# Kernel tuning notes

Measured on AMD Instinct MI355X. Metric: run time of the kernel, lower is better.

## Reference

```python
import jax, jax.numpy as jnp
import numpy as np

B, S, D, H, L, V = 2, 2048, 768, 12, 2, 32000
DH = D // H
DF = 4 * D
LN_EPS = 1e-5


def _pos_enc():
    # faithful to source: exponent uses 2*i/D with i already stepping by 2
    pos = jnp.arange(S, dtype=jnp.float32)[:, None]
    i = jnp.arange(0, D, 2, dtype=jnp.float32)
    ang = pos / (10000.0 ** (2.0 * i / D))
    enc = jnp.zeros((S, D), jnp.float32)
    enc = enc.at[:, 0::2].set(jnp.sin(ang)).at[:, 1::2].set(jnp.cos(ang))
    return enc


def _ln(x, g, b):
    m = jnp.mean(x, axis=-1, keepdims=True)
    v = jnp.mean((x - m) ** 2, axis=-1, keepdims=True)
    return (x - m) / jnp.sqrt(v + LN_EPS) * g + b


def _layer(x, p):
    Wq, bq, Wk, bk, Wv, bv, Wo, bo, g1, be1, W1, b1, W2, b2, g2, be2 = p
    q = (x @ Wq + bq).reshape(B, S, H, DH)
    k = (x @ Wk + bk).reshape(B, S, H, DH)
    v = (x @ Wv + bv).reshape(B, S, H, DH)
    # NOTE: source divides by sqrt(embed_dim), not sqrt(head_dim)
    attn = jnp.einsum('bqhd,bkhd->bhqk', q, k) / jnp.sqrt(jnp.float32(D))
    attn = jax.nn.softmax(attn, axis=-1)  # [B,H,S,S]
    o = jnp.einsum('bhqk,bkhd->bqhd', attn, v).reshape(B, S, D)
    o = o @ Wo + bo
    x = _ln(x + o, g1, be1)
    h = jax.nn.gelu(x @ W1 + b1, approximate=False)
    x = _ln(x + h @ W2 + b2, g2, be2)
    return x


def setup_inputs() -> dict:
    key = jax.random.key(0)
    ks = jax.random.split(key, 16)
    n = lambda k, shape: jax.random.normal(k, shape, dtype=jnp.float32) * 0.02
    return {
        'input_ids': jax.random.randint(ks[0], (B, S), 0, V),
        'embed_table': n(ks[1], (V, D)),
        'Wq': n(ks[2], (L, D, D)), 'bq': jnp.zeros((L, D), jnp.float32),
        'Wk': n(ks[3], (L, D, D)), 'bk': jnp.zeros((L, D), jnp.float32),
        'Wv': n(ks[4], (L, D, D)), 'bv': jnp.zeros((L, D), jnp.float32),
        'Wo': n(ks[5], (L, D, D)), 'bo': jnp.zeros((L, D), jnp.float32),
        'ln1_g': jnp.ones((L, D), jnp.float32), 'ln1_b': jnp.zeros((L, D), jnp.float32),
        'W1': n(ks[6], (L, D, DF)), 'b1': jnp.zeros((L, DF), jnp.float32),
        'W2': n(ks[7], (L, DF, D)), 'b2': jnp.zeros((L, D), jnp.float32),
        'ln2_g': jnp.ones((L, D), jnp.float32), 'ln2_b': jnp.zeros((L, D), jnp.float32),
        'Wd': n(ks[8], (D, D)), 'bd': jnp.zeros((D,), jnp.float32),
        'lnm_g': jnp.ones((D,), jnp.float32), 'lnm_b': jnp.zeros((D,), jnp.float32),
        'dec_b': jnp.zeros((V,), jnp.float32),
    }


def reference(input_ids, embed_table, Wq, bq, Wk, bk, Wv, bv, Wo, bo,
              ln1_g, ln1_b, W1, b1, W2, b2, ln2_g, ln2_b,
              Wd, bd, lnm_g, lnm_b, dec_b):
    x = embed_table[input_ids] + _pos_enc()[None]  # [B,S,D]

    def step(h, p):
        return _layer(h, p), None

    x, _ = jax.lax.scan(step, x, (Wq, bq, Wk, bk, Wv, bv, Wo, bo,
                                  ln1_g, ln1_b, W1, b1, W2, b2, ln2_g, ln2_b))
    # MLM head with decoder weight tied to embedding table
    h = jax.nn.gelu(x @ Wd + bd, approximate=False)
    h = _ln(h, lnm_g, lnm_b)
    return h @ embed_table.T + dec_b  # [B,S,V]
```

## Files before the change

kernel.cpp:

```cpp
#include <hip/hip_runtime.h>
#include <hip/hip_bf16.h>
#include <cstdint>

typedef __bf16 bf16x8 __attribute__((ext_vector_type(8)));
typedef float  f32x4  __attribute__((ext_vector_type(4)));
typedef unsigned short u16;
typedef u16 u16x8 __attribute__((ext_vector_type(8)));

__device__ __forceinline__ u16 f2bf(float f) {
    union { float f; uint32_t u; } x{f};
    uint32_t u = x.u;
    return (u16)((u + 0x7fffu + ((u >> 16) & 1u)) >> 16);
}

__device__ __forceinline__ float gelu_f(float x) {
    return 0.5f * x * (1.0f + erff(x * 0.70710678118654752f));
}

__device__ __forceinline__ void gl_lds16(const void* g, void* l) {
    __builtin_amdgcn_global_load_lds(
        (__attribute__((address_space(1))) void*)(void*)g,
        (__attribute__((address_space(3))) void*)l, 16, 0, 0);
}

#define MFMA16(a, b, c) __builtin_amdgcn_mfma_f32_16x16x32_bf16((a), (b), (c), 0, 0, 0)
#define SB0 __builtin_amdgcn_sched_barrier(0)

template<int EPI, int OUTF32, int LOC, int SPLITK>
__global__ __launch_bounds__(256, 2) void gemm_bf16(
    const u16* __restrict__ A, const u16* __restrict__ Bt,
    const float* __restrict__ bias, void* __restrict__ Cout,
    int N_, int K_)
{
    __shared__ u16 lA[128 * 64];
    __shared__ u16 lB[128 * 64];
    const int tid  = threadIdx.x;
    const int lane = tid & 63;
    const int wave = tid >> 6;
    const int wr = wave >> 1, wc = wave & 1;
    long row0, col0;
    if (LOC) {
        const int bid = blockIdx.x;
        const int chunk = bid >> 9, rem = bid & 511;
        row0 = (long)(rem & 31) * 128;
        col0 = (long)(chunk * 16 + (rem >> 5)) * 128;
    } else {
        row0 = (long)blockIdx.y * 128;
        col0 = (long)blockIdx.x * 128;
    }
    const int KS = K_ / SPLITK;
    const int kz = (SPLITK > 1) ? blockIdx.z * KS : 0;

    f32x4 acc[4][4];
#pragma unroll
    for (int i = 0; i < 4; ++i)
#pragma unroll
        for (int j = 0; j < 4; ++j)
#pragma unroll
            for (int t = 0; t < 4; ++t) acc[i][j][t] = 0.f;

    int sRow[4], sKb[4];
#pragma unroll
    for (int t = 0; t < 4; ++t) {
        int byteoff = (wave * 4 + t) * 1024 + lane * 16;
        int r = byteoff >> 7;
        sRow[t] = r;
        sKb[t]  = (byteoff & 127) ^ ((r & 7) << 4);
    }
    const int laneRC = lane & 15;
    const int laneK2 = (lane >> 4) * 16;

    for (int k0 = kz; k0 < kz + KS; k0 += 64) {
#pragma unroll
        for (int t = 0; t < 4; ++t) {
            const int cb = (wave * 4 + t) * 1024;
            gl_lds16(A  + (row0 + sRow[t]) * K_ + k0 + (sKb[t] >> 1), (char*)lA + cb);
            gl_lds16(Bt + (col0 + sRow[t]) * K_ + k0 + (sKb[t] >> 1), (char*)lB + cb);
        }
        __syncthreads();
#pragma unroll
        for (int kk = 0; kk < 2; ++kk) {
            bf16x8 af[4], bfr[4];
#pragma unroll
            for (int i = 0; i < 4; ++i) {
                int r = wr * 64 + i * 16 + laneRC;
                af[i] = *(const bf16x8*)((const char*)lA + r * 128 + ((kk * 64 + laneK2) ^ ((r & 7) << 4)));
            }
#pragma unroll
            for (int j = 0; j < 4; ++j) {
                int n = wc * 64 + j * 16 + laneRC;
                bfr[j] = *(const bf16x8*)((const char*)lB + n * 128 + ((kk * 64 + laneK2) ^ ((n & 7) << 4)));
            }
#pragma unroll
            for (int i = 0; i < 4; ++i)
#pragma unroll
                for (int j = 0; j < 4; ++j)
                    acc[i][j] = MFMA16(af[i], bfr[j], acc[i][j]);
        }
        __syncthreads();
    }

    float* outF = (float*)Cout + (SPLITK > 1 ? (long)blockIdx.z * 4096 * N_ : 0);
#pragma unroll
    for (int j = 0; j < 4; ++j) {
        const long cidx = col0 + wc * 64 + j * 16 + laneRC;
        const float bvv = (SPLITK == 1 || blockIdx.z == 0) ? bias[cidx] : 0.f;
#pragma unroll
        for (int i = 0; i < 4; ++i) {
            const long rbase = row0 + wr * 64 + i * 16 + ((lane >> 4) << 2);
#pragma unroll
            for (int t = 0; t < 4; ++t) {
                float v = acc[i][j][t] + bvv;
                if (EPI) v = gelu_f(v);
                const long off = (rbase + t) * N_ + cidx;
                if (OUTF32) outF[off] = v;
                else        ((u16*)Cout)[off] = f2bf(v);
            }
        }
    }
}

template<int EPI, int OUTF32>
__global__ __launch_bounds__(256, 4) void gemm64(
    const u16* __restrict__ A, const u16* __restrict__ Bt,
    const float* __restrict__ bias, void* __restrict__ Cout,
    int N_, int K_)
{
    __shared__ u16 lA[64 * 64];
    __shared__ u16 lB[64 * 64];
    const int tid  = threadIdx.x;
    const int lane = tid & 63;
    const int wave = tid >> 6;
    const int wr = wave >> 1, wc = wave & 1;
    const long row0 = (long)blockIdx.y * 64;
    const long col0 = (long)blockIdx.x * 64;

    f32x4 acc[2][2];
#pragma unroll
    for (int i = 0; i < 2; ++i)
#pragma unroll
        for (int j = 0; j < 2; ++j)
#pragma unroll
            for (int t = 0; t < 4; ++t) acc[i][j][t] = 0.f;

    int sRow[2], sKb[2];
#pragma unroll
    for (int t = 0; t < 2; ++t) {
        int byteoff = (wave * 2 + t) * 1024 + lane * 16;
        int r = byteoff >> 7;
        sRow[t] = r;
        sKb[t]  = (byteoff & 127) ^ ((r & 7) << 4);
    }
    const int laneRC = lane & 15;
    const int laneK2 = (lane >> 4) * 16;

    for (int k0 = 0; k0 < K_; k0 += 64) {
#pragma unroll
        for (int t = 0; t < 2; ++t) {
            const int cb = (wave * 2 + t) * 1024;
            gl_lds16(A  + (row0 + sRow[t]) * K_ + k0 + (sKb[t] >> 1), (char*)lA + cb);
            gl_lds16(Bt + (col0 + sRow[t]) * K_ + k0 + (sKb[t] >> 1), (char*)lB + cb);
        }
        __syncthreads();
#pragma unroll
        for (int kk = 0; kk < 2; ++kk) {
            bf16x8 af[2], bfr[2];
#pragma unroll
            for (int i = 0; i < 2; ++i) {
                int r = wr * 32 + i * 16 + laneRC;
                af[i] = *(const bf16x8*)((const char*)lA + r * 128 + ((kk * 64 + laneK2) ^ ((r & 7) << 4)));
            }
#pragma unroll
            for (int j = 0; j < 2; ++j) {
                int n = wc * 32 + j * 16 + laneRC;
                bfr[j] = *(const bf16x8*)((const char*)lB + n * 128 + ((kk * 64 + laneK2) ^ ((n & 7) << 4)));
            }
#pragma unroll
            for (int i = 0; i < 2; ++i)
#pragma unroll
                for (int j = 0; j < 2; ++j)
                    acc[i][j] = MFMA16(af[i], bfr[j], acc[i][j]);
        }
        __syncthreads();
    }

#pragma unroll
    for (int j = 0; j < 2; ++j) {
        const long cidx = col0 + wc * 32 + j * 16 + laneRC;
        const float bvv = bias[cidx];
#pragma unroll
        for (int i = 0; i < 2; ++i) {
            const long rbase = row0 + wr * 32 + i * 16 + ((lane >> 4) << 2);
#pragma unroll
            for (int t = 0; t < 4; ++t) {
                float v = acc[i][j][t] + bvv;
                if (EPI) v = gelu_f(v);
                const long off = (rbase + t) * N_ + cidx;
                if (OUTF32) ((float*)Cout)[off] = v;
                else        ((u16*)Cout)[off]  = f2bf(v);
            }
        }
    }
}

__global__ __launch_bounds__(256, 3) void attn_fwd(
    const u16* __restrict__ qkv, u16* __restrict__ outb, float scale)
{
    __shared__ u16 lQ[64 * 64];
    __shared__ u16 lK[2][64 * 64];
    __shared__ u16 lVt[2][64 * 64];
    __shared__ u16 lP[64 * 64];
    const int bh = blockIdx.x;
    const int b = bh / 12, h = bh % 12;
    const int q0 = blockIdx.y * 64;
    const int tid = threadIdx.x, lane = tid & 63, wave = tid >> 6;
    const long baseQ = (long)b * 2048 * 2304 + h * 64;
    const long baseK = baseQ + 768;
    const long baseV = baseQ + 1536;
    const int laneRC = lane & 15;
    const int laneK2 = (lane >> 4) * 16;

    int stR[2], stC[2];
#pragma unroll
    for (int t = 0; t < 2; ++t) {
        const int byteoff = (wave * 2 + t) * 1024 + lane * 16;
        const int r = byteoff >> 7;
        stR[t] = r;
        stC[t] = ((byteoff & 127) ^ ((r & 7) << 4)) >> 1;
    }

#define STAGEK(BUF, KB0) do {                                                    \
    _Pragma("unroll") for (int t = 0; t < 2; ++t)                                \
        gl_lds16(qkv + baseK + (long)((KB0) + stR[t]) * 2304 + stC[t],           \
                 (char*)lK[BUF] + (wave * 2 + t) * 1024);                        \
} while (0)

#pragma unroll
    for (int t = 0; t < 2; ++t)
        gl_lds16(qkv + baseQ + (long)(q0 + stR[t]) * 2304 + stC[t],
                 (char*)lQ + (wave * 2 + t) * 1024);
    STAGEK(0, 0);
    u16x8 vA0, vA1;
    {
        const u16x8* gv = (const u16x8*)(qkv + baseV + (long)lane * 2304 + wave * 16);
        vA0 = gv[0]; vA1 = gv[1];
    }
    __syncthreads();

    bf16x8 qf[2];
#pragma unroll
    for (int kk = 0; kk < 2; ++kk) {
        int r = wave * 16 + laneRC;
        qf[kk] = *(const bf16x8*)((const char*)lQ + r * 128 + ((kk * 64 + laneK2) ^ ((r & 7) << 4)));
    }

    bf16x8 onesf;
#pragma unroll
    for (int j = 0; j < 8; ++j) onesf[j] = (__bf16)1.0f;

    float mrun[4];
    f32x4 oacc[4], oaccS;
#pragma unroll
    for (int r = 0; r < 4; ++r) mrun[r] = -1e30f;
#pragma unroll
    for (int dc = 0; dc < 4; ++dc)
#pragma unroll
        for (int t = 0; t < 4; ++t) oacc[dc][t] = 0.f;
#pragma unroll
    for (int t = 0; t < 4; ++t) oaccS[t] = 0.f;

    u16x8 vB0 = vA0, vB1 = vA1;
    for (int kt = 0; kt < 32; ++kt) {
        const int cur = kt & 1;
        asm volatile("s_waitcnt vmcnt(0)" ::: "memory");
        SB0;
        {
            const int kv = lane, dg = wave;
            char* vt = (char*)lVt[cur];
#pragma unroll
            for (int j = 0; j < 8; ++j) {
                int d0 = dg * 16 + j;
                *(u16*)(vt + d0 * 128 + ((kv * 2) ^ ((d0 & 7) << 4))) = vA0[j];
                int d1 = dg * 16 + 8 + j;
                *(u16*)(vt + d1 * 128 + ((kv * 2) ^ ((d1 & 7) << 4))) = vA1[j];
            }
        }
        __builtin_amdgcn_s_barrier();
        SB0;
        if (kt + 1 < 32) {
            STAGEK(cur ^ 1, (kt + 1) * 64);
            const u16x8* gv = (const u16x8*)(qkv + baseV + (long)((kt + 1) * 64 + lane) * 2304 + wave * 16);
            vB0 = gv[0]; vB1 = gv[1];
        }
        const char* lKc = (const char*)lK[cur];
        const char* lVc = (const char*)lVt[cur];

        f32x4 s[4];
#pragma unroll
        for (int cb = 0; cb < 4; ++cb)
#pragma unroll
            for (int t = 0; t < 4; ++t) s[cb][t] = 0.f;
        __builtin_amdgcn_s_setprio(1);
#pragma unroll
        for (int kk = 0; kk < 2; ++kk) {
            bf16x8 kf[4];
#pragma unroll
            for (int cb = 0; cb < 4; ++cb) {
                int kr = cb * 16 + laneRC;
                kf[cb] = *(const bf16x8*)(lKc + kr * 128 + ((kk * 64 + laneK2) ^ ((kr & 7) << 4)));
            }
#pragma unroll
            for (int cb = 0; cb < 4; ++cb)
                s[cb] = MFMA16(qf[kk], kf[cb], s[cb]);
        }
        __builtin_amdgcn_s_setprio(0);

        if ((kt & 3) == 0) {
            float tm[4];
#pragma unroll
            for (int r = 0; r < 4; ++r) {
                float v = fmaxf(fmaxf(s[0][r], s[1][r]), fmaxf(s[2][r], s[3][r])) * scale;
#pragma unroll
                for (int msk = 1; msk < 16; msk <<= 1) v = fmaxf(v, __shfl_xor(v, msk, 64));
                tm[r] = v;
            }
            float ex = fmaxf(fmaxf(tm[0] - mrun[0], tm[1] - mrun[1]),
                             fmaxf(tm[2] - mrun[2], tm[3] - mrun[3]));
            if (__ballot(ex > 8.0f)) {
                float corr[4];
#pragma unroll
                for (int r = 0; r < 4; ++r) {
                    float mnew = fmaxf(mrun[r], tm[r]);
                    corr[r] = __expf(mrun[r] - mnew);
                    mrun[r] = mnew;
                }
                const int srcl = ((lane & 15) >> 2) << 4;
                float c0 = __shfl(corr[0], srcl, 64);
                float c1 = __shfl(corr[1], srcl, 64);
                float c2 = __shfl(corr[2], srcl, 64);
                float c3 = __shfl(corr[3], srcl, 64);
                const int selr = (lane & 15) & 3;
                float cp = selr == 0 ? c0 : (selr == 1 ? c1 : (selr == 2 ? c2 : c3));
#pragma unroll
                for (int dc = 0; dc < 4; ++dc)
#pragma unroll
                    for (int t = 0; t < 4; ++t) oacc[dc][t] *= cp;
#pragma unroll
                for (int t = 0; t < 4; ++t) oaccS[t] *= cp;
            }
        }
#pragma unroll
        for (int cb2 = 0; cb2 < 4; ++cb2) {
            int pcol = cb2 * 16 + laneRC;
#pragma unroll
            for (int r = 0; r < 4; ++r) {
                float pv = __expf(s[cb2][r] * scale - mrun[r]);
                int prow = wave * 16 + ((lane >> 4) << 2) + r;
                *(u16*)((char*)lP + prow * 128 + ((pcol * 2) ^ ((prow & 7) << 4))) = f2bf(pv);
            }
        }

        __builtin_amdgcn_s_setprio(1);
#pragma unroll
        for (int kk = 0; kk < 2; ++kk) {
            bf16x8 pf, vf[4];
            {
                int pr = wave * 16 + laneRC;
                pf = *(const bf16x8*)((const char*)lP + pr * 128 + ((kk * 64 + laneK2) ^ ((pr & 7) << 4)));
            }
#pragma unroll
            for (int dc = 0; dc < 4; ++dc) {
                int d = dc * 16 + laneRC;
                vf[dc] = *(const bf16x8*)(lVc + d * 128 + ((kk * 64 + laneK2) ^ ((d & 7) << 4)));
            }
#pragma unroll
            for (int dc = 0; dc < 4; ++dc)
                oacc[dc] = MFMA16(vf[dc], pf, oacc[dc]);
            oaccS = MFMA16(onesf, pf, oaccS);
        }
        __builtin_amdgcn_s_setprio(0);
        vA0 = vB0; vA1 = vB1;
    }
#undef STAGEK

    const float inv = 1.0f / oaccS[0];
    const long rowq = (long)b * 2048 + q0 + wave * 16 + (lane & 15);
#pragma unroll
    for (int dc = 0; dc < 4; ++dc) {
        const int colb = h * 64 + dc * 16 + ((lane >> 4) << 2);
        ushort4 st;
        st.x = f2bf(oacc[dc][0] * inv);
        st.y = f2bf(oacc[dc][1] * inv);
        st.z = f2bf(oacc[dc][2] * inv);
        st.w = f2bf(oacc[dc][3] * inv);
        *(ushort4*)(outb + rowq * 768 + colb) = st;
    }
}

template<int NP>
__global__ __launch_bounds__(256) void ln_fused(
    const float* __restrict__ a, const float* __restrict__ parts, long pstride,
    const float* __restrict__ g, const float* __restrict__ be,
    float* __restrict__ outf, u16* __restrict__ outb)
{
    const int wave = threadIdx.x >> 6, lane = threadIdx.x & 63;
    const int row = blockIdx.x * 4 + wave;
    const size_t rbase = (size_t)row * 768;
    float4 v[3];
    float s1 = 0.f, s2 = 0.f;
#pragma unroll
    for (int i = 0; i < 3; ++i) {
        const int c = lane * 4 + i * 256;
        float4 x = *(const float4*)(a + rbase + c);
#pragma unroll
        for (int p = 0; p < NP; ++p) {
            const float4 y = *(const float4*)(parts + (size_t)p * pstride + rbase + c);
            x.x += y.x; x.y += y.y; x.z += y.z; x.w += y.w;
        }
        v[i] = x;
        s1 += x.x + x.y + x.z + x.w;
        s2 += x.x * x.x + x.y * x.y + x.z * x.z + x.w * x.w;
    }
#pragma unroll
    for (int m = 1; m < 64; m <<= 1) { s1 += __shfl_xor(s1, m, 64); s2 += __shfl_xor(s2, m, 64); }
    const float mean = s1 * (1.f / 768.f);
    const float var  = s2 * (1.f / 768.f) - mean * mean;
    const float rstd = rsqrtf(var + 1e-5f);
#pragma unroll
    for (int i = 0; i < 3; ++i) {
        const int c = lane * 4 + i * 256;
        const float4 gg = *(const float4*)(g + c);
        const float4 bb = *(const float4*)(be + c);
        float4 y;
        y.x = (v[i].x - mean) * rstd * gg.x + bb.x;
        y.y = (v[i].y - mean) * rstd * gg.y + bb.y;
        y.z = (v[i].z - mean) * rstd * gg.z + bb.z;
        y.w = (v[i].w - mean) * rstd * gg.w + bb.w;
        if (outf) *(float4*)(outf + rbase + c) = y;
        ushort4 u; u.x = f2bf(y.x); u.y = f2bf(y.y); u.z = f2bf(y.z); u.w = f2bf(y.w);
        *(ushort4*)(outb + rbase + c) = u;
    }
}

struct TP9 { const float* s[9]; u16* d[9]; };
__global__ void transpose_multi(TP9 p, int R, int C)
{
    __shared__ float t[32][33];
    const float* in = p.s[blockIdx.z];
    u16* out = p.d[blockIdx.z];
    const int c0 = blockIdx.x * 32, r0 = blockIdx.y * 32;
    const int tx = threadIdx.x, ty = threadIdx.y;
#pragma unroll
    for (int i = 0; i < 4; ++i)
        t[ty + 8 * i][tx] = in[(size_t)(r0 + ty + 8 * i) * C + c0 + tx];
    __syncthreads();
#pragma unroll
    for (int i = 0; i < 4; ++i)
        out[(size_t)(c0 + ty + 8 * i) * R + r0 + tx] = f2bf(t[tx][ty + 8 * i]);
}

__global__ __launch_bounds__(256) void prep_misc(
    const float* __restrict__ emb, u16* __restrict__ embB,
    const int* __restrict__ ids, float* __restrict__ xf, u16* __restrict__ xb,
    const float* __restrict__ bq, const float* __restrict__ bk,
    const float* __restrict__ bv, float* __restrict__ bqkv)
{
    const long A = 6144000;
    const long B = 3145728;
    long t = (long)blockIdx.x * 256 + threadIdx.x;
    if (t < A) {
        const long i = t * 4;
        const float4 f = *(const float4*)(emb + i);
        ushort4 u; u.x = f2bf(f.x); u.y = f2bf(f.y); u.z = f2bf(f.z); u.w = f2bf(f.w);
        *(ushort4*)(embB + i) = u;
    } else if (t < A + B) {
        const int idx = (int)(t - A);
        const int row = idx / 768, d = idx - row * 768;
        const int s = row & 2047;
        const float e = emb[(long)ids[row] * 768 + d];
        const int j = d >> 1;
        const float ang = (float)s * __expf(-0.011992630692677324f * (float)(4 * j));
        const float pe = (d & 1) ? __cosf(ang) : __sinf(ang);
        const float v = e + pe;
        xf[idx] = v;
        xb[idx] = f2bf(v);
    } else {
        const int i = (int)(t - A - B);
        if (i < 4608) {
            int l = i / 2304, j = i - l * 2304;
            float v = (j < 768) ? bq[l * 768 + j]
                    : (j < 1536) ? bk[l * 768 + j - 768]
                    : bv[l * 768 + j - 1536];
            bqkv[i] = v;
        }
    }
}

extern "C" void kernel_launch(void* const* d_in, const int* in_sizes, int n_in,
                              void* d_out, int out_size, void* d_ws, size_t ws_size,
                              hipStream_t stream)
{
    const int S = 2048, D = 768, H = 12, L = 2, V = 32000, DF = 3072, M = 4096, NQKV = 2304;
    (void)in_sizes; (void)n_in; (void)out_size; (void)ws_size; (void)H; (void)S;

    const int*   ids  = (const int*)  d_in[0];
    const float* emb  = (const float*)d_in[1];
    const float* Wq   = (const float*)d_in[2];
    const float* bq   = (const float*)d_in[3];
    const float* Wk   = (const float*)d_in[4];
    const float* bk   = (const float*)d_in[5];
    const float* Wv   = (const float*)d_in[6];
    const float* bv   = (const float*)d_in[7];
    const float* Wo   = (const float*)d_in[8];
    const float* bo   = (const float*)d_in[9];
    const float* ln1g = (const float*)d_in[10];
    const float* ln1b = (const float*)d_in[11];
    const float* W1   = (const float*)d_in[12];
    const float* b1   = (const float*)d_in[13];
    const float* W2   = (const float*)d_in[14];
    const float* b2   = (const float*)d_in[15];
    const float* ln2g = (const float*)d_in[16];
    const float* ln2b = (const float*)d_in[17];
    const float* Wd   = (const float*)d_in[18];
    const float* bd   = (const float*)d_in[19];
    const float* lnmg = (const float*)d_in[20];
    const float* lnmb = (const float*)d_in[21];
    const float* decb = (const float*)d_in[22];

    char* p = (char*)d_ws;
    auto carve = [&](size_t bytes) { char* r = p; p += (bytes + 255) & ~(size_t)255; return r; };
    u16*   embB  = (u16*)  carve((size_t)V * D * 2);
    u16*   wqkvT = (u16*)  carve((size_t)L * NQKV * D * 2);
    float* bqkv  = (float*)carve((size_t)L * NQKV * 4);
    u16*   woT   = (u16*)  carve((size_t)L * D * D * 2);
    u16*   w1T   = (u16*)  carve((size_t)L * DF * D * 2);
    u16*   w2T   = (u16*)  carve((size_t)L * D * DF * 2);
    u16*   wdT   = (u16*)  carve((size_t)D * D * 2);
    float* xf    = (float*)carve((size_t)M * D * 4);
    u16*   xb    = (u16*)  carve((size_t)M * D * 2);
    u16*   qkvB  = (u16*)  carve((size_t)M * NQKV * 2);
    u16*   aoB   = (u16*)  carve((size_t)M * D * 2);
    float* tmpf  = (float*)carve((size_t)M * D * 4 * 4);
    u16*   hB    = (u16*)  carve((size_t)M * DF * 2);

    dim3 t32x8(32, 8);
    prep_misc<<<(6144000 + 3145728 + 4608) / 256, 256, 0, stream>>>(
        emb, embB, ids, xf, xb, bq, bk, bv, bqkv);
    {
        TP9 t9;
        for (int l = 0; l < L; ++l) {
            t9.s[l * 4 + 0] = Wq + (size_t)l * D * D; t9.d[l * 4 + 0] = wqkvT + (size_t)l * NQKV * D;
            t9.s[l * 4 + 1] = Wk + (size_t)l * D * D; t9.d[l * 4 + 1] = wqkvT + (size_t)l * NQKV * D + (size_t)D * D;
            t9.s[l * 4 + 2] = Wv + (size_t)l * D * D; t9.d[l * 4 + 2] = wqkvT + (size_t)l * NQKV * D + (size_t)2 * D * D;
            t9.s[l * 4 + 3] = Wo + (size_t)l * D * D; t9.d[l * 4 + 3] = woT + (size_t)l * D * D;
        }
        t9.s[8] = Wd; t9.d[8] = wdT;
        transpose_multi<<<dim3(24, 24, 9), t32x8, 0, stream>>>(t9, D, D);
        TP9 tw1; tw1.s[0] = W1; tw1.d[0] = w1T; tw1.s[1] = W1 + (size_t)D * DF; tw1.d[1] = w1T + (size_t)DF * D;
        transpose_multi<<<dim3(96, 24, 2), t32x8, 0, stream>>>(tw1, D, DF);
        TP9 tw2; tw2.s[0] = W2; tw2.d[0] = w2T; tw2.s[1] = W2 + (size_t)DF * D; tw2.d[1] = w2T + (size_t)D * DF;
        transpose_multi<<<dim3(24, 96, 2), t32x8, 0, stream>>>(tw2, DF, D);
    }

    const float scale = 0.036084391824351615f;
    const long PSTR = (long)M * D;
    for (int l = 0; l < L; ++l) {
        gemm_bf16<0, 0, 0, 1><<<dim3(NQKV / 128, M / 128), 256, 0, stream>>>(xb, wqkvT + (size_t)l * NQKV * D, bqkv + l * NQKV, qkvB, NQKV, D);
        attn_fwd<<<dim3(24, 32), 256, 0, stream>>>(qkvB, aoB, scale);
        gemm64<0, 1><<<dim3(D / 64, M / 64), 256, 0, stream>>>(aoB, woT + (size_t)l * D * D, bo + l * D, tmpf, D, D);
        ln_fused<1><<<M / 4, 256, 0, stream>>>(xf, tmpf, PSTR, ln1g + l * D, ln1b + l * D, xf, xb);
        gemm_bf16<1, 0, 0, 1><<<dim3(DF / 128, M / 128), 256, 0, stream>>>(xb, w1T + (size_t)l * DF * D, b1 + l * DF, hB, DF, D);
        gemm_bf16<0, 1, 0, 4><<<dim3(D / 128, M / 128, 4), 256, 0, stream>>>(hB, w2T + (size_t)l * D * DF, b2 + l * D, tmpf, D, DF);
        ln_fused<4><<<M / 4, 256, 0, stream>>>(xf, tmpf, PSTR, ln2g + l * D, ln2b + l * D, xf, xb);
    }
    gemm64<1, 1><<<dim3(D / 64, M / 64), 256, 0, stream>>>(xb, wdT, bd, tmpf, D, D);
    ln_fused<0><<<M / 4, 256, 0, stream>>>(tmpf, nullptr, 0, lnmg, lnmb, nullptr, aoB);
    gemm_bf16<0, 1, 1, 1><<<V / 128 * 32, 256, 0, stream>>>(aoB, embB, decb, (float*)d_out, V, D);
}
```

Before: 740.1 us.

## Merge prep kernels, share Q/P LDS buffer, raise attention occupancy, halve split-K

```diff
diff --git a/kernel.cpp b/kernel.cpp
--- a/kernel.cpp
+++ b/kernel.cpp
@@ -203,13 +203,12 @@
     }
 }
 
-__global__ __launch_bounds__(256, 3) void attn_fwd(
+__global__ __launch_bounds__(256, 4) void attn_fwd(
     const u16* __restrict__ qkv, u16* __restrict__ outb, float scale)
 {
-    __shared__ u16 lQ[64 * 64];
+    __shared__ u16 lQP[64 * 64];
     __shared__ u16 lK[2][64 * 64];
     __shared__ u16 lVt[2][64 * 64];
-    __shared__ u16 lP[64 * 64];
     const int bh = blockIdx.x;
     const int b = bh / 12, h = bh % 12;
     const int q0 = blockIdx.y * 64;
@@ -238,7 +237,7 @@
 #pragma unroll
     for (int t = 0; t < 2; ++t)
         gl_lds16(qkv + baseQ + (long)(q0 + stR[t]) * 2304 + stC[t],
-                 (char*)lQ + (wave * 2 + t) * 1024);
+                 (char*)lQP + (wave * 2 + t) * 1024);
     STAGEK(0, 0);
     u16x8 vA0, vA1;
     {
@@ -251,7 +250,7 @@
 #pragma unroll
     for (int kk = 0; kk < 2; ++kk) {
         int r = wave * 16 + laneRC;
-        qf[kk] = *(const bf16x8*)((const char*)lQ + r * 128 + ((kk * 64 + laneK2) ^ ((r & 7) << 4)));
+        qf[kk] = *(const bf16x8*)((const char*)lQP + r * 128 + ((kk * 64 + laneK2) ^ ((r & 7) << 4)));
     }
 
     bf16x8 onesf;
@@ -315,7 +314,7 @@
         }
         __builtin_amdgcn_s_setprio(0);
 
-        if ((kt & 3) == 0) {
+        if ((kt & 7) == 0) {
             float tm[4];
 #pragma unroll
             for (int r = 0; r < 4; ++r) {
@@ -356,7 +355,7 @@
             for (int r = 0; r < 4; ++r) {
                 float pv = __expf(s[cb2][r] * scale - mrun[r]);
                 int prow = wave * 16 + ((lane >> 4) << 2) + r;
-                *(u16*)((char*)lP + prow * 128 + ((pcol * 2) ^ ((prow & 7) << 4))) = f2bf(pv);
+                *(u16*)((char*)lQP + prow * 128 + ((pcol * 2) ^ ((prow & 7) << 4))) = f2bf(pv);
             }
         }
 
@@ -366,7 +365,7 @@
             bf16x8 pf, vf[4];
             {
                 int pr = wave * 16 + laneRC;
-                pf = *(const bf16x8*)((const char*)lP + pr * 128 + ((kk * 64 + laneK2) ^ ((pr & 7) << 4)));
+                pf = *(const bf16x8*)((const char*)lQP + pr * 128 + ((kk * 64 + laneK2) ^ ((pr & 7) << 4)));
             }
 #pragma unroll
             for (int dc = 0; dc < 4; ++dc) {
@@ -442,56 +441,61 @@
     }
 }
 
-struct TP9 { const float* s[9]; u16* d[9]; };
-__global__ void transpose_multi(TP9 p, int R, int C)
+struct PrepArgs {
+    const float* tsrc[13]; u16* tdst[13];
+    const float* emb; u16* embB;
+    const int* ids; float* xf; u16* xb;
+    const float* bq; const float* bk; const float* bv; float* bqkv;
+};
+__global__ __launch_bounds__(256) void prep_all(PrepArgs pa)
 {
-    __shared__ float t[32][33];
-    const float* in = p.s[blockIdx.z];
-    u16* out = p.d[blockIdx.z];
-    const int c0 = blockIdx.x * 32, r0 = blockIdx.y * 32;
-    const int tx = threadIdx.x, ty = threadIdx.y;
-#pragma unroll
-    for (int i = 0; i < 4; ++i)
-        t[ty + 8 * i][tx] = in[(size_t)(r0 + ty + 8 * i) * C + c0 + tx];
-    __syncthreads();
-#pragma unroll
-    for (int i = 0; i < 4; ++i)
-        out[(size_t)(c0 + ty + 8 * i) * R + r0 + tx] = f2bf(t[tx][ty + 8 * i]);
-}
-
-__global__ __launch_bounds__(256) void prep_misc(
-    const float* __restrict__ emb, u16* __restrict__ embB,
-    const int* __restrict__ ids, float* __restrict__ xf, u16* __restrict__ xb,
-    const float* __restrict__ bq, const float* __restrict__ bk,
-    const float* __restrict__ bv, float* __restrict__ bqkv)
-{
+    const int bid = blockIdx.x;
+    if (bid < 14400) {
+        int z, bx, by, R, C;
+        if (bid < 5184)       { z = bid / 576;              int r = bid - z * 576;    bx = r % 24; by = r / 24; R = 768;  C = 768;  }
+        else if (bid < 9792)  { z = 9 + (bid - 5184) / 2304;  int r = (bid - 5184) % 2304; bx = r % 96; by = r / 96; R = 768;  C = 3072; }
+        else                  { z = 11 + (bid - 9792) / 2304; int r = (bid - 9792) % 2304; bx = r % 24; by = r / 24; R = 3072; C = 768;  }
+        __shared__ float t[32][33];
+        const float* in = pa.tsrc[z];
+        u16* out = pa.tdst[z];
+        const int c0 = bx * 32, r0 = by * 32;
+        const int tx = threadIdx.x & 31, ty = threadIdx.x >> 5;
+#pragma unroll
+        for (int i = 0; i < 4; ++i)
+            t[ty + 8 * i][tx] = in[(size_t)(r0 + ty + 8 * i) * C + c0 + tx];
+        __syncthreads();
+#pragma unroll
+        for (int i = 0; i < 4; ++i)
+            out[(size_t)(c0 + ty + 8 * i) * R + r0 + tx] = f2bf(t[tx][ty + 8 * i]);
+        return;
+    }
     const long A = 6144000;
     const long B = 3145728;
-    long t = (long)blockIdx.x * 256 + threadIdx.x;
+    long t = (long)(bid - 14400) * 256 + threadIdx.x;
     if (t < A) {
         const long i = t * 4;
-        const float4 f = *(const float4*)(emb + i);
+        const float4 f = *(const float4*)(pa.emb + i);
         ushort4 u; u.x = f2bf(f.x); u.y = f2bf(f.y); u.z = f2bf(f.z); u.w = f2bf(f.w);
-        *(ushort4*)(embB + i) = u;
+        *(ushort4*)(pa.embB + i) = u;
     } else if (t < A + B) {
         const int idx = (int)(t - A);
         const int row = idx / 768, d = idx - row * 768;
         const int s = row & 2047;
-        const float e = emb[(long)ids[row] * 768 + d];
+        const float e = pa.emb[(long)pa.ids[row] * 768 + d];
         const int j = d >> 1;
         const float ang = (float)s * __expf(-0.011992630692677324f * (float)(4 * j));
         const float pe = (d & 1) ? __cosf(ang) : __sinf(ang);
         const float v = e + pe;
-        xf[idx] = v;
-        xb[idx] = f2bf(v);
+        pa.xf[idx] = v;
+        pa.xb[idx] = f2bf(v);
     } else {
         const int i = (int)(t - A - B);
         if (i < 4608) {
             int l = i / 2304, j = i - l * 2304;
-            float v = (j < 768) ? bq[l * 768 + j]
-                    : (j < 1536) ? bk[l * 768 + j - 768]
-                    : bv[l * 768 + j - 1536];
-            bqkv[i] = v;
+            float v = (j < 768) ? pa.bq[l * 768 + j]
+                    : (j < 1536) ? pa.bk[l * 768 + j - 768]
+                    : pa.bv[l * 768 + j - 1536];
+            pa.bqkv[i] = v;
         }
     }
 }
@@ -543,23 +547,23 @@
     float* tmpf  = (float*)carve((size_t)M * D * 4 * 4);
     u16*   hB    = (u16*)  carve((size_t)M * DF * 2);
 
-    dim3 t32x8(32, 8);
-    prep_misc<<<(6144000 + 3145728 + 4608) / 256, 256, 0, stream>>>(
-        emb, embB, ids, xf, xb, bq, bk, bv, bqkv);
     {
-        TP9 t9;
+        PrepArgs pa;
         for (int l = 0; l < L; ++l) {
-            t9.s[l * 4 + 0] = Wq + (size_t)l * D * D; t9.d[l * 4 + 0] = wqkvT + (size_t)l * NQKV * D;
-            t9.s[l * 4 + 1] = Wk + (size_t)l * D * D; t9.d[l * 4 + 1] = wqkvT + (size_t)l * NQKV * D + (size_t)D * D;
-            t9.s[l * 4 + 2] = Wv + (size_t)l * D * D; t9.d[l * 4 + 2] = wqkvT + (size_t)l * NQKV * D + (size_t)2 * D * D;
-            t9.s[l * 4 + 3] = Wo + (size_t)l * D * D; t9.d[l * 4 + 3] = woT + (size_t)l * D * D;
-        }
-        t9.s[8] = Wd; t9.d[8] = wdT;
-        transpose_multi<<<dim3(24, 24, 9), t32x8, 0, stream>>>(t9, D, D);
-        TP9 tw1; tw1.s[0] = W1; tw1.d[0] = w1T; tw1.s[1] = W1 + (size_t)D * DF; tw1.d[1] = w1T + (size_t)DF * D;
-        transpose_multi<<<dim3(96, 24, 2), t32x8, 0, stream>>>(tw1, D, DF);
-        TP9 tw2; tw2.s[0] = W2; tw2.d[0] = w2T; tw2.s[1] = W2 + (size_t)DF * D; tw2.d[1] = w2T + (size_t)D * DF;
-        transpose_multi<<<dim3(24, 96, 2), t32x8, 0, stream>>>(tw2, DF, D);
+            pa.tsrc[l * 4 + 0] = Wq + (size_t)l * D * D; pa.tdst[l * 4 + 0] = wqkvT + (size_t)l * NQKV * D;
+            pa.tsrc[l * 4 + 1] = Wk + (size_t)l * D * D; pa.tdst[l * 4 + 1] = wqkvT + (size_t)l * NQKV * D + (size_t)D * D;
+            pa.tsrc[l * 4 + 2] = Wv + (size_t)l * D * D; pa.tdst[l * 4 + 2] = wqkvT + (size_t)l * NQKV * D + (size_t)2 * D * D;
+            pa.tsrc[l * 4 + 3] = Wo + (size_t)l * D * D; pa.tdst[l * 4 + 3] = woT + (size_t)l * D * D;
+        }
+        pa.tsrc[8]  = Wd;                    pa.tdst[8]  = wdT;
+        pa.tsrc[9]  = W1;                    pa.tdst[9]  = w1T;
+        pa.tsrc[10] = W1 + (size_t)D * DF;   pa.tdst[10] = w1T + (size_t)DF * D;
+        pa.tsrc[11] = W2;                    pa.tdst[11] = w2T;
+        pa.tsrc[12] = W2 + (size_t)DF * D;   pa.tdst[12] = w2T + (size_t)D * DF;
+        pa.emb = emb; pa.embB = embB;
+        pa.ids = ids; pa.xf = xf; pa.xb = xb;
+        pa.bq = bq; pa.bk = bk; pa.bv = bv; pa.bqkv = bqkv;
+        prep_all<<<14400 + 36306, 256, 0, stream>>>(pa);
     }
 
     const float scale = 0.036084391824351615f;
@@ -570,8 +574,8 @@
         gemm64<0, 1><<<dim3(D / 64, M / 64), 256, 0, stream>>>(aoB, woT + (size_t)l * D * D, bo + l * D, tmpf, D, D);
         ln_fused<1><<<M / 4, 256, 0, stream>>>(xf, tmpf, PSTR, ln1g + l * D, ln1b + l * D, xf, xb);
         gemm_bf16<1, 0, 0, 1><<<dim3(DF / 128, M / 128), 256, 0, stream>>>(xb, w1T + (size_t)l * DF * D, b1 + l * DF, hB, DF, D);
-        gemm_bf16<0, 1, 0, 4><<<dim3(D / 128, M / 128, 4), 256, 0, stream>>>(hB, w2T + (size_t)l * D * DF, b2 + l * D, tmpf, D, DF);
-        ln_fused<4><<<M / 4, 256, 0, stream>>>(xf, tmpf, PSTR, ln2g + l * D, ln2b + l * D, xf, xb);
+        gemm_bf16<0, 1, 0, 2><<<dim3(D / 128, M / 128, 2), 256, 0, stream>>>(hB, w2T + (size_t)l * D * DF, b2 + l * D, tmpf, D, DF);
+        ln_fused<2><<<M / 4, 256, 0, stream>>>(xf, tmpf, PSTR, ln2g + l * D, ln2b + l * D, xf, xb);
     }
     gemm64<1, 1><<<dim3(D / 64, M / 64), 256, 0, stream>>>(xb, wdT, bd, tmpf, D, D);
     ln_fused<0><<<M / 4, 256, 0, stream>>>(tmpf, nullptr, 0, lnmg, lnmb, nullptr, aoB);
```

After: 719.2 us. -2.8%, faster.
